# Performance work log

Measured on AMD Instinct MI355X. Metric: run time of the kernel, lower is better.

Reference implementation:

```python
import jax, jax.numpy as jnp
import numpy as np


def setup_inputs() -> dict:
    key = jax.random.key(0)
    ks = jax.random.split(key, 5)
    B, Tm1, N, H = 128, 255, 256, 256  # batch, t-1, input_size, hidden_encoder
    X = jax.random.normal(ks[0], (B, Tm1, N), dtype=jnp.float32)
    W_attn = jax.random.normal(ks[1], (2 * H + Tm1, 1), dtype=jnp.float32) * 0.05
    b_attn = jnp.zeros((1,), dtype=jnp.float32)
    W_lstm = jax.random.normal(ks[2], (N, 4 * H), dtype=jnp.float32) * 0.05
    U_lstm = jax.random.normal(ks[3], (H, 4 * H), dtype=jnp.float32) * 0.05
    b_lstm = jnp.zeros((4 * H,), dtype=jnp.float32)
    return {"X": X, "W_attn": W_attn, "b_attn": b_attn,
            "W_lstm": W_lstm, "U_lstm": U_lstm, "b_lstm": b_lstm}


def reference(X, W_attn, b_attn, W_lstm, U_lstm, b_lstm):
    B, Tm1, N = X.shape
    H = U_lstm.shape[0]
    # init_state: RepeatVector(H)(X[:,0,:])[:,:,0] == X[:,0,0] tiled across hidden
    h0 = jnp.broadcast_to(X[:, 0, 0:1], (B, H))
    c0 = h0
    Xp = jnp.transpose(X, (0, 2, 1))  # (B, N, Tm1), reused every step

    def step(carry, x_t):  # x_t: (B, N) = X[:, t, :]
        h, c = carry
        # encoder_concat: (B, N, 2H + Tm1)
        feat = jnp.concatenate([
            jnp.broadcast_to(h[:, None, :], (B, N, H)),
            jnp.broadcast_to(c[:, None, :], (B, N, H)),
            Xp,
        ], axis=2)
        e = jnp.einsum('bnf,fo->bno', feat, W_attn)[..., 0] + b_attn[0]  # (B, N)
        alpha = jax.nn.softmax(e, axis=-1)  # softmax over input_size
        x_tilde = alpha * x_t  # (B, N)
        # Keras LSTM cell, gate order [i, f, g, o]
        z = x_tilde @ W_lstm + h @ U_lstm + b_lstm  # (B, 4H)
        i, f, g, o = jnp.split(z, 4, axis=-1)
        i = jax.nn.sigmoid(i)
        f = jax.nn.sigmoid(f)
        g = jnp.tanh(g)
        o = jax.nn.sigmoid(o)
        c_new = f * c + i * g
        h_new = o * jnp.tanh(c_new)
        return (h_new, c_new), (x_tilde, h_new)

    (_, _), (X_tilde, X_encoded) = jax.lax.scan(step, (h0, c0),
                                                jnp.transpose(X, (1, 0, 2)))
    X_tilde = jnp.transpose(X_tilde, (1, 0, 2))    # (B, Tm1, N)
    X_encoded = jnp.transpose(X_encoded, (1, 0, 2))  # (B, Tm1, H)
    return X_tilde, X_encoded
```

## Files before the change

kernel.cpp:

```cpp
#include <hip/hip_runtime.h>
#include <hip/hip_bf16.h>
#include <stdint.h>

#define B_ 128
#define T_ 255
#define N_ 256
#define H_ 256

#define RP_ 92
#define LQ_ 9

typedef _Float16 f16;
typedef _Float16 f16x2 __attribute__((ext_vector_type(2)));
typedef _Float16 f16x8 __attribute__((ext_vector_type(8)));
typedef float f32x4 __attribute__((ext_vector_type(4)));

static __device__ __forceinline__ float fdot2(uint32_t h, uint32_t u, float acc) {
#if __has_builtin(__builtin_amdgcn_fdot2)
  return __builtin_amdgcn_fdot2(__builtin_bit_cast(f16x2, h),
                                __builtin_bit_cast(f16x2, u), acc, false);
#else
  f16x2 a = __builtin_bit_cast(f16x2, h);
  f16x2 b = __builtin_bit_cast(f16x2, u);
  return acc + (float)a.x * (float)b.x + (float)a.y * (float)b.y;
#endif
}

__global__ __launch_bounds__(256) void k0_pack(const float* __restrict__ Wl,
                                               const float* __restrict__ Ul,
                                               uint32_t* __restrict__ u_packed,
                                               f16* __restrict__ wt) {
  int idx = blockIdx.x * 256 + threadIdx.x;
  if (idx < 256 * 1024) {
    int n = idx >> 8, k = idx & 255;
    wt[n * 256 + k] = (f16)Wl[k * 1024 + n];
  }
  if (idx < 128 * 1024) {
    int p = idx >> 10, c = idx & 1023;
    f16x2 v;
    v.x = (f16)Ul[(2 * p) * 1024 + c];
    v.y = (f16)Ul[(2 * p + 1) * 1024 + c];
    u_packed[idx] = __builtin_bit_cast(uint32_t, v);
  }
}

__global__ __launch_bounds__(256) void k1_alpha(const float* __restrict__ X,
                                                const float* __restrict__ Wa,
                                                float* __restrict__ alpha) {
  int b = blockIdx.x, n = threadIdx.x;
  const float* xb = X + b * (T_ * N_) + n;
  float a0 = 0.f, a1 = 0.f, a2 = 0.f, a3 = 0.f;
  int t = 0;
  for (; t + 4 <= T_; t += 4) {
    a0 += xb[(t + 0) * N_] * Wa[512 + t + 0];
    a1 += xb[(t + 1) * N_] * Wa[512 + t + 1];
    a2 += xb[(t + 2) * N_] * Wa[512 + t + 2];
    a3 += xb[(t + 3) * N_] * Wa[512 + t + 3];
  }
  for (; t < T_; ++t) a0 += xb[t * N_] * Wa[512 + t];
  float e = (a0 + a1) + (a2 + a3);

  __shared__ float red[4];
  float m = e;
  for (int off = 32; off > 0; off >>= 1) m = fmaxf(m, __shfl_xor(m, off));
  int wid = n >> 6;
  if ((n & 63) == 0) red[wid] = m;
  __syncthreads();
  m = fmaxf(fmaxf(red[0], red[1]), fmaxf(red[2], red[3]));
  float ex = __expf(e - m);
  float s = ex;
  for (int off = 32; off > 0; off >>= 1) s += __shfl_xor(s, off);
  __syncthreads();
  if ((n & 63) == 0) red[wid] = s;
  __syncthreads();
  s = (red[0] + red[1]) + (red[2] + red[3]);
  alpha[b * N_ + n] = ex / s;
}

__global__ __launch_bounds__(256) void k2_xtilde(const float4* __restrict__ X4,
                                                 const float* __restrict__ alpha,
                                                 float4* __restrict__ out4) {
  int i = blockIdx.x * 256 + threadIdx.x;
  if (i < B_ * T_ * 64) {
    int n4 = i & 63;
    int bt = i >> 6;
    int b = bt / T_;
    const float4* A4 = (const float4*)alpha;
    float4 x = X4[i], al = A4[b * 64 + n4];
    float4 r;
    r.x = x.x * al.x; r.y = x.y * al.y; r.z = x.z * al.z; r.w = x.w * al.w;
    out4[i] = r;
  }
}

#define LDA 40
__global__ __launch_bounds__(256, 2) void k3_gemm(const float* __restrict__ A,
                                                  const f16* __restrict__ Bt,
                                                  const float* __restrict__ bias,
                                                  f16* __restrict__ Cw) {
  __shared__ f16 As[128 * LDA];
  __shared__ f16 Bs[128 * LDA];
  int tid = threadIdx.x;
  int mt = blockIdx.x;
  int nt = blockIdx.y;
  int lane = tid & 63, wid = tid >> 6;
  int wm = (wid >> 1) * 64, wn = (wid & 1) * 64;
  f32x4 acc[4][4] = {};

  for (int k0 = 0; k0 < 256; k0 += 32) {
    __syncthreads();
#pragma unroll
    for (int it = 0; it < 4; ++it) {
      int idx = tid + it * 256;
      int r = idx >> 3, q = idx & 7;
      float4 v = *(const float4*)(A + (mt * 128 + r) * 256 + k0 + q * 4);
      f16x2 p0, p1;
      p0.x = (f16)v.x; p0.y = (f16)v.y; p1.x = (f16)v.z; p1.y = (f16)v.w;
      uint2 w;
      w.x = __builtin_bit_cast(uint32_t, p0);
      w.y = __builtin_bit_cast(uint32_t, p1);
      *(uint2*)(&As[r * LDA + q * 4]) = w;
    }
#pragma unroll
    for (int it = 0; it < 2; ++it) {
      int idx = tid + it * 256;
      int r = idx >> 2, q = idx & 3;
      uint4 v = *(const uint4*)(Bt + (nt * 128 + r) * 256 + k0 + q * 8);
      *(uint4*)(&Bs[r * LDA + q * 8]) = v;
    }
    __syncthreads();
    int kb = (lane >> 4) * 8;
    f16x8 af[4], bf[4];
#pragma unroll
    for (int i = 0; i < 4; ++i)
      af[i] = *(const f16x8*)(&As[(wm + i * 16 + (lane & 15)) * LDA + kb]);
#pragma unroll
    for (int j = 0; j < 4; ++j)
      bf[j] = *(const f16x8*)(&Bs[(wn + j * 16 + (lane & 15)) * LDA + kb]);
#pragma unroll
    for (int i = 0; i < 4; ++i)
#pragma unroll
      for (int j = 0; j < 4; ++j)
        acc[i][j] = __builtin_amdgcn_mfma_f32_16x16x32_f16(af[i], bf[j], acc[i][j], 0, 0, 0);
  }
  int colL = wn + (lane & 15);
  int rowB = wm + (lane >> 4) * 4;
#pragma unroll
  for (int j = 0; j < 4; ++j) {
    int ng = nt * 128 + colL + j * 16;
    float bv = bias[ng];
#pragma unroll
    for (int i = 0; i < 4; ++i)
#pragma unroll
      for (int r = 0; r < 4; ++r) {
        int mg = mt * 128 + rowB + i * 16 + r;
        Cw[mg * 1024 + ng] = (f16)(acc[i][j][r] + bv);
      }
  }
}

__global__ __launch_bounds__(1024) void k4_recur(const float* __restrict__ X,
                                                 const uint32_t* __restrict__ u_packed,
                                                 const f16* __restrict__ xwf,
                                                 float* __restrict__ Xenc) {
  __shared__ __align__(16) uint32_t u_lds[LQ_ * 1024 * 4];
  __shared__ __align__(16) f16 h_lds[256];
  __shared__ __align__(16) float z_lds[1024];
  int tid = threadIdx.x, b = blockIdx.x;

  uint32_t ur[RP_];
#pragma unroll
  for (int p = 0; p < RP_; ++p) ur[p] = u_packed[p * 1024 + tid];

  {
    uint4* dst = (uint4*)u_lds;
#pragma unroll
    for (int q = 0; q < LQ_; ++q) {
      int base = (RP_ + 4 * q) * 1024 + tid;
      uint4 v;
      v.x = u_packed[base];
      v.y = u_packed[base + 1024];
      v.z = u_packed[base + 2048];
      v.w = u_packed[base + 3072];
      dst[q * 1024 + tid] = v;
    }
  }
  float x00 = X[b * (T_ * N_)];
  float c_st = x00;
  if (tid < 256) h_lds[tid] = (f16)x00;
  __syncthreads();

  const f16* xwb = xwf + (size_t)b * T_ * 1024;
  float* encb = Xenc + (size_t)b * T_ * N_;
  const uint4* h4 = (const uint4*)h_lds;
  const uint4* u4 = (const uint4*)u_lds;

  float xwv = (float)xwb[tid];
  for (int t = 0; t < T_; ++t) {
    float xw_nxt = 0.f;
    if (t + 1 < T_) xw_nxt = (float)xwb[(t + 1) * 1024 + tid];

    float za = xwv, zb = 0.f;
#pragma unroll
    for (int q = 0; q < RP_ / 4; ++q) {
      uint4 hh = h4[q];
      za = fdot2(hh.x, ur[4 * q + 0], za);
      zb = fdot2(hh.y, ur[4 * q + 1], zb);
      za = fdot2(hh.z, ur[4 * q + 2], za);
      zb = fdot2(hh.w, ur[4 * q + 3], zb);
    }
#pragma unroll
    for (int q = 0; q < LQ_; ++q) {
      uint4 hh = h4[RP_ / 4 + q];
      uint4 uu = u4[q * 1024 + tid];
      za = fdot2(hh.x, uu.x, za);
      zb = fdot2(hh.y, uu.y, zb);
      za = fdot2(hh.z, uu.z, za);
      zb = fdot2(hh.w, uu.w, zb);
    }
    z_lds[tid] = za + zb;
    __syncthreads();
    if (tid < 256) {
      float zi = z_lds[tid], zf = z_lds[256 + tid];
      float zg = z_lds[512 + tid], zo = z_lds[768 + tid];
      float ig = 1.f / (1.f + __expf(-zi));
      float fg = 1.f / (1.f + __expf(-zf));
      float gg = 1.f - 2.f / (1.f + __expf(2.f * zg));
      float og = 1.f / (1.f + __expf(-zo));
      c_st = fg * c_st + ig * gg;
      float hv = og * (1.f - 2.f / (1.f + __expf(2.f * c_st)));
      encb[t * 256 + tid] = hv;
      h_lds[tid] = (f16)hv;
    }
    __syncthreads();
    xwv = xw_nxt;
  }
}

extern "C" void kernel_launch(void* const* d_in, const int* in_sizes, int n_in,
                              void* d_out, int out_size, void* d_ws, size_t ws_size,
                              hipStream_t stream) {
  const float* X = (const float*)d_in[0];
  const float* Wa = (const float*)d_in[1];
  const float* Wl = (const float*)d_in[3];
  const float* Ul = (const float*)d_in[4];
  const float* bl = (const float*)d_in[5];
  float* out = (float*)d_out;
  uint8_t* ws = (uint8_t*)d_ws;

  float* alpha = (float*)ws;
  uint32_t* u_packed = (uint32_t*)(ws + 131072);
  f16* wt = (f16*)(ws + 655360);
  f16* xw = (f16*)(ws + 1179648);

  k0_pack<<<1024, 256, 0, stream>>>(Wl, Ul, u_packed, wt);
  k1_alpha<<<128, 256, 0, stream>>>(X, Wa, alpha);
  k2_xtilde<<<8160, 256, 0, stream>>>((const float4*)X, alpha, (float4*)out);
  dim3 g3(255, 8);
  k3_gemm<<<g3, 256, 0, stream>>>(out, wt, bl, xw);
  k4_recur<<<128, 1024, 0, stream>>>(X, u_packed, xw, out + 8355840);
}
```

Measured before the change: 659.3 us.

## Use MFMA for recurrent h@U matvec with register/LDS-split U fragments

The recurrent kernel now computes the per-step h·U product with 16x16x32 f16 MFMA instructions instead of per-thread fdot2 chains. U is repacked into MFMA A-fragment layout, with most fragments held in registers (loaded via inline asm) and the rest in LDS. The block shrinks to 512 threads (8 waves). Only one column of the B operand is meaningful, so most MFMA work is wasted, but it replaces 128 dot instructions per thread with fewer matrix ops. The risk is register pressure from 46 uint4 fragments and higher per-step latency on the serial path.

```diff
diff --git a/kernel.cpp b/kernel.cpp
--- a/kernel.cpp
+++ b/kernel.cpp
@@ -7,40 +7,30 @@
 #define N_ 256
 #define H_ 256
 
-#define RP_ 92
-#define LQ_ 9
-
 typedef _Float16 f16;
 typedef _Float16 f16x2 __attribute__((ext_vector_type(2)));
 typedef _Float16 f16x8 __attribute__((ext_vector_type(8)));
 typedef float f32x4 __attribute__((ext_vector_type(4)));
 
-static __device__ __forceinline__ float fdot2(uint32_t h, uint32_t u, float acc) {
-#if __has_builtin(__builtin_amdgcn_fdot2)
-  return __builtin_amdgcn_fdot2(__builtin_bit_cast(f16x2, h),
-                                __builtin_bit_cast(f16x2, u), acc, false);
-#else
-  f16x2 a = __builtin_bit_cast(f16x2, h);
-  f16x2 b = __builtin_bit_cast(f16x2, u);
-  return acc + (float)a.x * (float)b.x + (float)a.y * (float)b.y;
-#endif
-}
-
 __global__ __launch_bounds__(256) void k0_pack(const float* __restrict__ Wl,
                                                const float* __restrict__ Ul,
-                                               uint32_t* __restrict__ u_packed,
+                                               uint32_t* __restrict__ um,
                                                f16* __restrict__ wt) {
   int idx = blockIdx.x * 256 + threadIdx.x;
   if (idx < 256 * 1024) {
     int n = idx >> 8, k = idx & 255;
     wt[n * 256 + k] = (f16)Wl[k * 1024 + n];
   }
-  if (idx < 128 * 1024) {
-    int p = idx >> 10, c = idx & 1023;
+  if (idx < 131072) {
+    int d = idx;
+    int w = d >> 14, f = (d >> 8) & 63, L = (d >> 2) & 63, ep = d & 3;
+    int j = f >> 3, q = f & 7;
+    int r0 = 32 * q + ((L >> 4) << 3) + 2 * ep;
+    int c = 128 * w + 16 * j + (L & 15);
     f16x2 v;
-    v.x = (f16)Ul[(2 * p) * 1024 + c];
-    v.y = (f16)Ul[(2 * p + 1) * 1024 + c];
-    u_packed[idx] = __builtin_bit_cast(uint32_t, v);
+    v.x = (f16)Ul[r0 * 1024 + c];
+    v.y = (f16)Ul[(r0 + 1) * 1024 + c];
+    um[d] = __builtin_bit_cast(uint32_t, v);
   }
 }
 
@@ -159,66 +149,83 @@
   }
 }
 
-__global__ __launch_bounds__(1024) void k4_recur(const float* __restrict__ X,
-                                                 const uint32_t* __restrict__ u_packed,
-                                                 const f16* __restrict__ xwf,
-                                                 float* __restrict__ Xenc) {
-  __shared__ __align__(16) uint32_t u_lds[LQ_ * 1024 * 4];
+#define UL4(F) uint4 a##F; \
+  asm volatile("global_load_dwordx4 %0, %1, off" : "=v"(a##F) \
+               : "v"(um4 + ((w * 64 + (F)) * 64 + L)));
+
+#define MR(J, F, Q) acc##J = __builtin_amdgcn_mfma_f32_16x16x32_f16( \
+    __builtin_bit_cast(f16x8, a##F), b##Q, acc##J, 0, 0, 0);
+#define ML(J, FL, Q) acc##J = __builtin_amdgcn_mfma_f32_16x16x32_f16( \
+    *(const f16x8*)(u_lds4 + (wl18 + (FL)) * 64 + L), b##Q, acc##J, 0, 0, 0);
+
+#define BQ(Q) f16x8 b##Q = *(const f16x8*)&h_lds[32 * (Q) + hoff];
+#define XLD(J) uint2 l##J = *(const uint2*)(xt + 16 * (J));
+#define AINIT(J) f32x4 acc##J; { \
+  f16x2 lo = __builtin_bit_cast(f16x2, l##J.x); \
+  f16x2 hi = __builtin_bit_cast(f16x2, l##J.y); \
+  acc##J[0] = (float)lo.x; acc##J[1] = (float)lo.y; \
+  acc##J[2] = (float)hi.x; acc##J[3] = (float)hi.y; }
+#define ZST(J) *(f32x4*)&z_lds[colbase + 16 * (J)] = acc##J;
+
+__global__ __launch_bounds__(512)
+void k4_recur(const float* __restrict__ X,
+              const uint4* __restrict__ um4,
+              const f16* __restrict__ xwf,
+              float* __restrict__ Xenc) {
+  __shared__ __align__(16) uint4 u_lds4[8 * 18 * 64];
   __shared__ __align__(16) f16 h_lds[256];
   __shared__ __align__(16) float z_lds[1024];
   int tid = threadIdx.x, b = blockIdx.x;
-
-  uint32_t ur[RP_];
-#pragma unroll
-  for (int p = 0; p < RP_; ++p) ur[p] = u_packed[p * 1024 + tid];
-
-  {
-    uint4* dst = (uint4*)u_lds;
-#pragma unroll
-    for (int q = 0; q < LQ_; ++q) {
-      int base = (RP_ + 4 * q) * 1024 + tid;
-      uint4 v;
-      v.x = u_packed[base];
-      v.y = u_packed[base + 1024];
-      v.z = u_packed[base + 2048];
-      v.w = u_packed[base + 3072];
-      dst[q * 1024 + tid] = v;
-    }
-  }
+  int w = tid >> 6, L = tid & 63;
+  int wl18 = w * 18;
+  int hoff = (L >> 4) << 3;
+  int colbase = 128 * w + ((L >> 4) << 2);
+
+  UL4(0)  UL4(1)  UL4(2)  UL4(3)  UL4(4)  UL4(5)  UL4(6)  UL4(7)
+  UL4(8)  UL4(9)  UL4(10) UL4(11) UL4(12) UL4(13) UL4(14) UL4(15)
+  UL4(16) UL4(17) UL4(18) UL4(19) UL4(20) UL4(21) UL4(22) UL4(23)
+  UL4(24) UL4(25) UL4(26) UL4(27) UL4(28) UL4(29) UL4(30) UL4(31)
+  UL4(32) UL4(33) UL4(34) UL4(35) UL4(36) UL4(37) UL4(38) UL4(39)
+  UL4(40) UL4(41) UL4(42) UL4(43) UL4(44) UL4(45)
+
+#pragma unroll
+  for (int f = 46; f < 64; ++f)
+    u_lds4[(wl18 + f - 46) * 64 + L] = um4[(w * 64 + f) * 64 + L];
+
   float x00 = X[b * (T_ * N_)];
   float c_st = x00;
   if (tid < 256) h_lds[tid] = (f16)x00;
+  asm volatile("s_waitcnt vmcnt(0)" ::: "memory");
   __syncthreads();
 
   const f16* xwb = xwf + (size_t)b * T_ * 1024;
   float* encb = Xenc + (size_t)b * T_ * N_;
-  const uint4* h4 = (const uint4*)h_lds;
-  const uint4* u4 = (const uint4*)u_lds;
-
-  float xwv = (float)xwb[tid];
+
   for (int t = 0; t < T_; ++t) {
-    float xw_nxt = 0.f;
-    if (t + 1 < T_) xw_nxt = (float)xwb[(t + 1) * 1024 + tid];
-
-    float za = xwv, zb = 0.f;
-#pragma unroll
-    for (int q = 0; q < RP_ / 4; ++q) {
-      uint4 hh = h4[q];
-      za = fdot2(hh.x, ur[4 * q + 0], za);
-      zb = fdot2(hh.y, ur[4 * q + 1], zb);
-      za = fdot2(hh.z, ur[4 * q + 2], za);
-      zb = fdot2(hh.w, ur[4 * q + 3], zb);
-    }
-#pragma unroll
-    for (int q = 0; q < LQ_; ++q) {
-      uint4 hh = h4[RP_ / 4 + q];
-      uint4 uu = u4[q * 1024 + tid];
-      za = fdot2(hh.x, uu.x, za);
-      zb = fdot2(hh.y, uu.y, zb);
-      za = fdot2(hh.z, uu.z, za);
-      zb = fdot2(hh.w, uu.w, zb);
-    }
-    z_lds[tid] = za + zb;
+    const f16* xt = xwb + t * 1024 + colbase;
+    XLD(0) XLD(1) XLD(2) XLD(3) XLD(4) XLD(5) XLD(6) XLD(7)
+    AINIT(0) AINIT(1) AINIT(2) AINIT(3) AINIT(4) AINIT(5) AINIT(6) AINIT(7)
+
+    BQ(0)
+    BQ(1)
+    MR(0,0,0)  MR(1,8,0)  MR(2,16,0) MR(3,24,0) MR(4,32,0) MR(5,40,0) ML(6,2,0)  ML(7,10,0)
+    BQ(2)
+    MR(0,1,1)  MR(1,9,1)  MR(2,17,1) MR(3,25,1) MR(4,33,1) MR(5,41,1) ML(6,3,1)  ML(7,11,1)
+    BQ(3)
+    MR(0,2,2)  MR(1,10,2) MR(2,18,2) MR(3,26,2) MR(4,34,2) MR(5,42,2) ML(6,4,2)  ML(7,12,2)
+    BQ(4)
+    MR(0,3,3)  MR(1,11,3) MR(2,19,3) MR(3,27,3) MR(4,35,3) MR(5,43,3) ML(6,5,3)  ML(7,13,3)
+    BQ(5)
+    MR(0,4,4)  MR(1,12,4) MR(2,20,4) MR(3,28,4) MR(4,36,4) MR(5,44,4) ML(6,6,4)  ML(7,14,4)
+    BQ(6)
+    MR(0,5,5)  MR(1,13,5) MR(2,21,5) MR(3,29,5) MR(4,37,5) MR(5,45,5) ML(6,7,5)  ML(7,15,5)
+    BQ(7)
+    MR(0,6,6)  MR(1,14,6) MR(2,22,6) MR(3,30,6) MR(4,38,6) ML(5,0,6)  ML(6,8,6)  ML(7,16,6)
+    MR(0,7,7)  MR(1,15,7) MR(2,23,7) MR(3,31,7) MR(4,39,7) ML(5,1,7)  ML(6,9,7)  ML(7,17,7)
+
+    if ((L & 15) == 0) {
+      ZST(0) ZST(1) ZST(2) ZST(3) ZST(4) ZST(5) ZST(6) ZST(7)
+    }
     __syncthreads();
     if (tid < 256) {
       float zi = z_lds[tid], zf = z_lds[256 + tid];
@@ -233,7 +240,6 @@
       h_lds[tid] = (f16)hv;
     }
     __syncthreads();
-    xwv = xw_nxt;
   }
 }
 
@@ -249,14 +255,15 @@
   uint8_t* ws = (uint8_t*)d_ws;
 
   float* alpha = (float*)ws;
-  uint32_t* u_packed = (uint32_t*)(ws + 131072);
+  uint32_t* u_mfma = (uint32_t*)(ws + 131072);
   f16* wt = (f16*)(ws + 655360);
   f16* xw = (f16*)(ws + 1179648);
 
-  k0_pack<<<1024, 256, 0, stream>>>(Wl, Ul, u_packed, wt);
+  k0_pack<<<1024, 256, 0, stream>>>(Wl, Ul, u_mfma, wt);
   k1_alpha<<<128, 256, 0, stream>>>(X, Wa, alpha);
   k2_xtilde<<<8160, 256, 0, stream>>>((const float4*)X, alpha, (float4*)out);
   dim3 g3(255, 8);
   k3_gemm<<<g3, 256, 0, stream>>>(out, wt, bl, xw);
-  k4_recur<<<128, 1024, 0, stream>>>(X, u_packed, xw, out + 8355840);
-}
+  k4_recur<<<128, 512, 0, stream>>>(X, (const uint4*)u_mfma, xw,
+                                    out + 8355840);
+}
```

Result: slower. 692.5 us (+5.0%).
